# Kernel optimization log

Hardware: AMD Instinct MI355X
Metric: run time of the kernel (lower is better)

Reference implementation:

```python
import jax, jax.numpy as jnp
import numpy as np

DIM = 1024
EPS = 1e-12  # torch F.normalize eps


def setup_inputs() -> dict:
    key = jax.random.key(0)
    k1, k2, k3 = jax.random.split(key, 3)
    b, n, d = 2, 4096, DIM
    x = jax.random.normal(k1, (b, n, d), dtype=jnp.float32)
    # nn.Linear(dim, 3*dim, bias=False): weight shape [3*dim, dim]
    w_qkva = jax.random.normal(k2, (3 * d, d), dtype=jnp.float32) * (1.0 / np.sqrt(d))
    gamma = jnp.ones((d,), dtype=jnp.float32)  # RMSNorm gamma (init ones)
    return {"x": x, "gamma": gamma, "w_qkva": w_qkva}


def _rmsnorm(x, gamma):
    # lucidrains RMSNorm: F.normalize(x, dim=-1) * sqrt(dim) * gamma
    norm = jnp.sqrt(jnp.sum(x * x, axis=-1, keepdims=True))
    scale = jnp.asarray(np.sqrt(x.shape[-1]), x.dtype)
    return x / jnp.maximum(norm, EPS) * scale * gamma


def reference(x, gamma, w_qkva):
    d = x.shape[-1]
    xn = _rmsnorm(x, gamma)
    qkva = jnp.einsum('bnd,ed->bne', xn, w_qkva)  # [b, n, 3d]
    q, kv, a = qkva[..., :d], qkva[..., d:2 * d], qkva[..., 2 * d:]
    a = jax.nn.sigmoid(a)

    def binary_operator(e_i, e_j):
        a_i, kv_i = e_i
        a_j, kv_j = e_j
        return a_j * a_i, a_j * kv_i + kv_j

    # per-channel scalar linear recurrence: kv_t = a_t * kv_{t-1} + kv_t
    _, kv_scan = jax.lax.associative_scan(binary_operator, (a, kv), axis=1)
    return q * kv_scan  # [b, n, d]
```

## Files before the change

### kernel.cpp

```cpp
#include <hip/hip_runtime.h>
#include <cstdint>
#include <cstddef>

#define DIMD 1024
#define BB 2
#define NN 4096
#define MM (BB*NN)
#define EE (3*DIMD)
#define KK DIMD

typedef __attribute__((ext_vector_type(8))) short short8;
typedef __attribute__((ext_vector_type(4))) float f32x4;

__device__ __forceinline__ unsigned short f2bf(float f) {
  unsigned int u = __float_as_uint(f);
  u += 0x7FFF + ((u >> 16) & 1);
  return (unsigned short)(u >> 16);
}

__global__ void cast_w_kernel(const float* __restrict__ w, unsigned short* __restrict__ wb) {
  int i = blockIdx.x * blockDim.x + threadIdx.x;
  const float4* w4 = (const float4*)w;
  float4 v = w4[i];
  unsigned int lo = (unsigned int)f2bf(v.x) | ((unsigned int)f2bf(v.y) << 16);
  unsigned int hi = (unsigned int)f2bf(v.z) | ((unsigned int)f2bf(v.w) << 16);
  ((uint2*)wb)[i] = make_uint2(lo, hi);
}

__global__ void rmsnorm_kernel(const float* __restrict__ x, const float* __restrict__ gamma,
                               unsigned short* __restrict__ xn) {
  int row = blockIdx.x;
  int tid = threadIdx.x;
  const float4* x4 = (const float4*)(x + (size_t)row * DIMD);
  float4 v = x4[tid];
  float ss = v.x*v.x + v.y*v.y + v.z*v.z + v.w*v.w;
  #pragma unroll
  for (int m = 32; m >= 1; m >>= 1) ss += __shfl_xor(ss, m);
  __shared__ float red[4];
  if ((tid & 63) == 0) red[tid >> 6] = ss;
  __syncthreads();
  float tot = red[0] + red[1] + red[2] + red[3];
  float scale = 32.0f / fmaxf(sqrtf(tot), 1e-12f);
  const float4* g4 = (const float4*)gamma;
  float4 g = g4[tid];
  float a0 = v.x*scale*g.x, a1 = v.y*scale*g.y, a2 = v.z*scale*g.z, a3 = v.w*scale*g.w;
  unsigned int lo = (unsigned int)f2bf(a0) | ((unsigned int)f2bf(a1) << 16);
  unsigned int hi = (unsigned int)f2bf(a2) | ((unsigned int)f2bf(a3) << 16);
  ((uint2*)(xn + (size_t)row * DIMD))[tid] = make_uint2(lo, hi);
}

#define BM 128
#define BN 128
#define BK 64

__global__ __launch_bounds__(256) void gemm_kernel(const unsigned short* __restrict__ A,
                                                   const unsigned short* __restrict__ Bw,
                                                   float* __restrict__ C) {
  __shared__ unsigned short Al[BM][BK];
  __shared__ unsigned short Bl[BN][BK];
  int tid = threadIdx.x;
  int l = tid & 63;
  int w = tid >> 6;
  int wr = w >> 1, wc = w & 1;
  int m0 = blockIdx.y * BM;
  int n0 = blockIdx.x * BN;
  int lrow = l & 15, lk = l >> 4;

  f32x4 acc[4][4];
  #pragma unroll
  for (int i = 0; i < 4; i++)
    #pragma unroll
    for (int j = 0; j < 4; j++) acc[i][j] = (f32x4)(0.f);

  for (int k0 = 0; k0 < KK; k0 += BK) {
    short8 ar[4], br[4];
    #pragma unroll
    for (int j = 0; j < 4; j++) {
      int cid = j*256 + tid;
      int row = cid >> 3, cb = cid & 7;
      ar[j] = *(const short8*)(A  + (size_t)(m0 + row)*KK + k0 + cb*8);
      br[j] = *(const short8*)(Bw + (size_t)(n0 + row)*KK + k0 + cb*8);
    }
    __syncthreads();
    #pragma unroll
    for (int j = 0; j < 4; j++) {
      int cid = j*256 + tid;
      int row = cid >> 3, cb = cid & 7;
      *(short8*)&Al[row][(cb ^ (row & 7)) * 8] = ar[j];
      *(short8*)&Bl[row][(cb ^ (row & 7)) * 8] = br[j];
    }
    __syncthreads();
    #pragma unroll
    for (int s = 0; s < 2; s++) {
      short8 af[4], bf[4];
      #pragma unroll
      for (int i = 0; i < 4; i++) {
        int r = wr*64 + i*16 + lrow;
        af[i] = *(const short8*)&Al[r][((s*4 + lk) ^ (r & 7)) * 8];
      }
      #pragma unroll
      for (int j = 0; j < 4; j++) {
        int r = wc*64 + j*16 + lrow;
        bf[j] = *(const short8*)&Bl[r][((s*4 + lk) ^ (r & 7)) * 8];
      }
      #pragma unroll
      for (int i = 0; i < 4; i++)
        #pragma unroll
        for (int j = 0; j < 4; j++)
          acc[i][j] = __builtin_amdgcn_mfma_f32_16x16x32_bf16(af[i], bf[j], acc[i][j], 0, 0, 0);
    }
  }

  #pragma unroll
  for (int i = 0; i < 4; i++) {
    int rowb = m0 + wr*64 + i*16 + lk*4;
    #pragma unroll
    for (int j = 0; j < 4; j++) {
      int col = n0 + wc*64 + j*16 + lrow;
      f32x4 v = acc[i][j];
      bool isg = (col >= 2*DIMD);
      #pragma unroll
      for (int r = 0; r < 4; r++) {
        float val = v[r];
        if (isg) val = 1.0f / (1.0f + __expf(-val));
        C[(size_t)(rowb + r)*EE + col] = val;
      }
    }
  }
}

#define CHUNK 128
#define NCH (NN / CHUNK)

__global__ void scan1_kernel(const float* __restrict__ qkva,
                             float* __restrict__ Aagg, float* __restrict__ Kagg) {
  int d = blockIdx.x * 256 + threadIdx.x;
  int c = blockIdx.y;
  int b = blockIdx.z;
  const float* p = qkva + ((size_t)(b*NN + c*CHUNK)) * EE;
  float Aa = 1.f, Kv = 0.f;
  for (int i = 0; i < CHUNK; i++) {
    float a  = p[2*DIMD + d];
    float kv = p[DIMD + d];
    Kv = fmaf(a, Kv, kv);
    Aa *= a;
    p += EE;
  }
  int idx = (b*NCH + c)*DIMD + d;
  Aagg[idx] = Aa;
  Kagg[idx] = Kv;
}

__global__ void scan2_kernel(const float* __restrict__ Aagg, const float* __restrict__ Kagg,
                             float* __restrict__ carry) {
  int t = blockIdx.x * 256 + threadIdx.x;
  int b = t >> 10, d = t & (DIMD - 1);
  float cy = 0.f;
  for (int c = 0; c < NCH; c++) {
    int idx = (b*NCH + c)*DIMD + d;
    carry[idx] = cy;
    cy = fmaf(Aagg[idx], cy, Kagg[idx]);
  }
}

__global__ void scan3_kernel(const float* __restrict__ qkva, const float* __restrict__ carry,
                             float* __restrict__ out) {
  int d = blockIdx.x * 256 + threadIdx.x;
  int c = blockIdx.y;
  int b = blockIdx.z;
  const float* p = qkva + ((size_t)(b*NN + c*CHUNK)) * EE;
  float* o = out + ((size_t)(b*NN + c*CHUNK)) * DIMD;
  float Kv = carry[(b*NCH + c)*DIMD + d];
  for (int i = 0; i < CHUNK; i++) {
    float a  = p[2*DIMD + d];
    float kv = p[DIMD + d];
    float q  = p[d];
    Kv = fmaf(a, Kv, kv);
    o[d] = q * Kv;
    p += EE;
    o += DIMD;
  }
}

extern "C" void kernel_launch(void* const* d_in, const int* in_sizes, int n_in,
                              void* d_out, int out_size, void* d_ws, size_t ws_size,
                              hipStream_t stream) {
  const float* x     = (const float*)d_in[0];
  const float* gamma = (const float*)d_in[1];
  const float* wq    = (const float*)d_in[2];
  float* out = (float*)d_out;
  char* ws = (char*)d_ws;

  unsigned short* Wb = (unsigned short*)ws;
  unsigned short* Xn = (unsigned short*)(ws + 6291456);
  float* qkva        = (float*)(ws + 23068672);
  float* Aagg        = (float*)(ws + 123731968);
  float* Kagg        = (float*)(ws + 123994112);
  float* carry       = (float*)(ws + 124256256);

  cast_w_kernel<<<(EE*KK)/(256*4), 256, 0, stream>>>(wq, Wb);
  rmsnorm_kernel<<<MM, 256, 0, stream>>>(x, gamma, Xn);
  gemm_kernel<<<dim3(EE/BN, MM/BM), 256, 0, stream>>>(Xn, Wb, qkva);
  scan1_kernel<<<dim3(DIMD/256, NCH, BB), 256, 0, stream>>>(qkva, Aagg, Kagg);
  scan2_kernel<<<dim3((BB*DIMD)/256), 256, 0, stream>>>(Aagg, Kagg, carry);
  scan3_kernel<<<dim3(DIMD/256, NCH, BB), 256, 0, stream>>>(qkva, carry, out);
}
```

Measured before the change: 224.9 us.

## Use direct global-to-LDS loads in GEMM and batch loads in scan kernels

The GEMM tile staging switches from loading into registers and then storing to LDS over to global_load_lds, which writes straight into shared memory with a matching XOR swizzle on the source column. The three scan kernels now issue eight rows of loads before running the dependent recurrence, so more memory requests are in flight per thread. The aim is to cut register staging and VGPR pressure in the GEMM and hide latency in the bandwidth-bound scans. The swizzle mapping for the direct LDS writes must match the read pattern exactly, or results will be wrong.

```diff
diff --git a/kernel.cpp b/kernel.cpp
--- a/kernel.cpp
+++ b/kernel.cpp
@@ -17,6 +17,10 @@
   u += 0x7FFF + ((u >> 16) & 1);
   return (unsigned short)(u >> 16);
 }
+
+#define GLOAD_LDS16(gptr, lptr) \
+  __builtin_amdgcn_global_load_lds((const __attribute__((address_space(1))) void*)(gptr), \
+                                   (__attribute__((address_space(3))) void*)(lptr), 16, 0, 0)
 
 __global__ void cast_w_kernel(const float* __restrict__ w, unsigned short* __restrict__ wb) {
   int i = blockIdx.x * blockDim.x + threadIdx.x;
@@ -66,6 +70,9 @@
   int n0 = blockIdx.x * BN;
   int lrow = l & 15, lk = l >> 4;
 
+  int srow_base = w * 32 + (l >> 3);
+  int scol = (((l & 7) ^ (l >> 3)) * 8);
+
   f32x4 acc[4][4];
   #pragma unroll
   for (int i = 0; i < 4; i++)
@@ -73,21 +80,12 @@
     for (int j = 0; j < 4; j++) acc[i][j] = (f32x4)(0.f);
 
   for (int k0 = 0; k0 < KK; k0 += BK) {
-    short8 ar[4], br[4];
-    #pragma unroll
-    for (int j = 0; j < 4; j++) {
-      int cid = j*256 + tid;
-      int row = cid >> 3, cb = cid & 7;
-      ar[j] = *(const short8*)(A  + (size_t)(m0 + row)*KK + k0 + cb*8);
-      br[j] = *(const short8*)(Bw + (size_t)(n0 + row)*KK + k0 + cb*8);
-    }
     __syncthreads();
     #pragma unroll
-    for (int j = 0; j < 4; j++) {
-      int cid = j*256 + tid;
-      int row = cid >> 3, cb = cid & 7;
-      *(short8*)&Al[row][(cb ^ (row & 7)) * 8] = ar[j];
-      *(short8*)&Bl[row][(cb ^ (row & 7)) * 8] = br[j];
+    for (int t = 0; t < 4; t++) {
+      int row = srow_base + t * 8;
+      GLOAD_LDS16(A  + (size_t)(m0 + row) * KK + k0 + scol, &Al[w*32 + t*8][0]);
+      GLOAD_LDS16(Bw + (size_t)(n0 + row) * KK + k0 + scol, &Bl[w*32 + t*8][0]);
     }
     __syncthreads();
     #pragma unroll
@@ -139,12 +137,14 @@
   int b = blockIdx.z;
   const float* p = qkva + ((size_t)(b*NN + c*CHUNK)) * EE;
   float Aa = 1.f, Kv = 0.f;
-  for (int i = 0; i < CHUNK; i++) {
-    float a  = p[2*DIMD + d];
-    float kv = p[DIMD + d];
-    Kv = fmaf(a, Kv, kv);
-    Aa *= a;
-    p += EE;
+  for (int i0 = 0; i0 < CHUNK; i0 += 8) {
+    float av[8], kvv[8];
+    #pragma unroll
+    for (int u = 0; u < 8; u++) av[u]  = p[(size_t)(i0+u)*EE + 2*DIMD + d];
+    #pragma unroll
+    for (int u = 0; u < 8; u++) kvv[u] = p[(size_t)(i0+u)*EE + DIMD + d];
+    #pragma unroll
+    for (int u = 0; u < 8; u++) { Kv = fmaf(av[u], Kv, kvv[u]); Aa *= av[u]; }
   }
   int idx = (b*NCH + c)*DIMD + d;
   Aagg[idx] = Aa;
@@ -156,10 +156,18 @@
   int t = blockIdx.x * 256 + threadIdx.x;
   int b = t >> 10, d = t & (DIMD - 1);
   float cy = 0.f;
-  for (int c = 0; c < NCH; c++) {
-    int idx = (b*NCH + c)*DIMD + d;
-    carry[idx] = cy;
-    cy = fmaf(Aagg[idx], cy, Kagg[idx]);
+  for (int c0 = 0; c0 < NCH; c0 += 8) {
+    float Av[8], Kv[8];
+    #pragma unroll
+    for (int u = 0; u < 8; u++) {
+      int idx = (b*NCH + c0 + u)*DIMD + d;
+      Av[u] = Aagg[idx]; Kv[u] = Kagg[idx];
+    }
+    #pragma unroll
+    for (int u = 0; u < 8; u++) {
+      carry[(b*NCH + c0 + u)*DIMD + d] = cy;
+      cy = fmaf(Av[u], cy, Kv[u]);
+    }
   }
 }
 
@@ -171,14 +179,19 @@
   const float* p = qkva + ((size_t)(b*NN + c*CHUNK)) * EE;
   float* o = out + ((size_t)(b*NN + c*CHUNK)) * DIMD;
   float Kv = carry[(b*NCH + c)*DIMD + d];
-  for (int i = 0; i < CHUNK; i++) {
-    float a  = p[2*DIMD + d];
-    float kv = p[DIMD + d];
-    float q  = p[d];
-    Kv = fmaf(a, Kv, kv);
-    o[d] = q * Kv;
-    p += EE;
-    o += DIMD;
+  for (int i0 = 0; i0 < CHUNK; i0 += 8) {
+    float av[8], kvv[8], qv[8];
+    #pragma unroll
+    for (int u = 0; u < 8; u++) av[u]  = p[(size_t)(i0+u)*EE + 2*DIMD + d];
+    #pragma unroll
+    for (int u = 0; u < 8; u++) kvv[u] = p[(size_t)(i0+u)*EE + DIMD + d];
+    #pragma unroll
+    for (int u = 0; u < 8; u++) qv[u]  = p[(size_t)(i0+u)*EE + d];
+    #pragma unroll
+    for (int u = 0; u < 8; u++) {
+      Kv = fmaf(av[u], Kv, kvv[u]);
+      o[(size_t)(i0+u)*DIMD + d] = qv[u] * Kv;
+    }
   }
 }
 
```

After: 209.4 us. -6.9%, faster.
